# Performance work log

Measured on AMD Instinct MI355X. Metric: run time of the kernel, lower is better.

Reference implementation:

```python
import jax, jax.numpy as jnp
import numpy as np


def setup_inputs() -> dict:
    key = jax.random.key(0)
    k1, k2 = jax.random.split(key)
    B, C, H, W, K = 4, 3, 720, 1280, 5
    data = jax.random.normal(k1, (B, C, H, W), dtype=jnp.float32)
    kernels = jax.random.normal(k2, (B, K * K, H, W), dtype=jnp.float32)
    return {"data": data, "kernels": kernels}


def reference(data, kernels):
    # data: [B, C, H, W]; kernels: [B, K*K, H, W]
    bs, k2, h, w = kernels.shape
    k = int(np.sqrt(k2))
    r = k // 2
    # softmax-normalize the K*K weights per pixel (dim=1 in the torch module)
    kern = jax.nn.softmax(kernels, axis=1).reshape(bs, k, k, h, w)
    # zero-pad data so out-of-bound neighbors contribute 0 (matches skipped
    # out-of-range taps in the CUDA kernel_weighting op)
    pad = jnp.pad(data, ((0, 0), (0, 0), (r, r), (r, r)))
    out = jnp.zeros_like(data)
    # fixed small K*K loop (25 taps); each tap is a shifted slice * per-pixel weight
    for i in range(k):
        for j in range(k):
            out = out + pad[:, :, i:i + h, j:j + w] * kern[:, i, j][:, None, :, :]
    return out
```

## Files before the change

kernel.cpp:

```cpp
#include <hip/hip_runtime.h>
#include <math.h>

#define BB 4
#define CC 3
#define HH 720
#define WW 1280
#define KS 5
#define KK 25
#define RR 2

__global__ __launch_bounds__(256) void kpn_weighting_kernel(
    const float* __restrict__ data,
    const float* __restrict__ kern,
    float* __restrict__ out)
{
    const int HW = HH * WW;
    int idx = blockIdx.x * blockDim.x + threadIdx.x;
    const int total = BB * HW;
    if (idx >= total) return;

    int b  = idx / HW;
    int hw = idx - b * HW;
    int h  = hw / WW;
    int w  = hw - h * WW;

    const float* kp = kern + (size_t)b * KK * HW + hw;
    float wt[KK];
    float m = -1e30f;
    #pragma unroll
    for (int t = 0; t < KK; ++t) {
        wt[t] = kp[(size_t)t * HW];
        m = fmaxf(m, wt[t]);
    }
    float s = 0.f;
    #pragma unroll
    for (int t = 0; t < KK; ++t) {
        wt[t] = __expf(wt[t] - m);
        s += wt[t];
    }
    float inv = 1.0f / s;
    #pragma unroll
    for (int t = 0; t < KK; ++t) wt[t] *= inv;

    #pragma unroll
    for (int c = 0; c < CC; ++c) {
        const float* dp = data + ((size_t)b * CC + c) * HW;
        float acc = 0.f;
        #pragma unroll
        for (int i = 0; i < KS; ++i) {
            int hh = h + i - RR;
            if (hh < 0 || hh >= HH) continue;
            const float* rowp = dp + (size_t)hh * WW;
            #pragma unroll
            for (int j = 0; j < KS; ++j) {
                int ww = w + j - RR;
                if (ww < 0 || ww >= WW) continue;
                acc = fmaf(rowp[ww], wt[i * KS + j], acc);
            }
        }
        out[((size_t)b * CC + c) * HW + hw] = acc;
    }
}

extern "C" void kernel_launch(void* const* d_in, const int* in_sizes, int n_in,
                              void* d_out, int out_size, void* d_ws, size_t ws_size,
                              hipStream_t stream) {
    const float* data = (const float*)d_in[0];
    const float* kern = (const float*)d_in[1];
    float* out = (float*)d_out;

    const int total = BB * HH * WW;
    const int block = 256;
    const int grid = (total + block - 1) / block;
    kpn_weighting_kernel<<<grid, block, 0, stream>>>(data, kern, out);
}
```

Before: 626.4 us.

## Process four pixels per thread with float4 loads and nontemporal kernel streaming

Each thread now handles four adjacent output pixels. It loads the 25 softmax logits as float4 nontemporal loads and reads each data row as three float4 vectors covering a 12-wide window, with zero fill at the image edges. Outputs go out as nontemporal float4 stores. The aim is fewer, wider memory transactions on a bandwidth-bound stencil, and less cache pollution from the single-use kernel tensor, at the cost of higher register pressure (100 weight registers per thread) and a quarter as many threads.

```diff
diff --git a/kernel.cpp b/kernel.cpp
--- a/kernel.cpp
+++ b/kernel.cpp
@@ -8,57 +8,89 @@
 #define KS 5
 #define KK 25
 #define RR 2
+#define W4 (WW / 4)
+#define HW (HH * WW)
 
-__global__ __launch_bounds__(256) void kpn_weighting_kernel(
+typedef float f4 __attribute__((ext_vector_type(4)));
+
+__global__ __launch_bounds__(256) void kpn_weighting_v4(
     const float* __restrict__ data,
     const float* __restrict__ kern,
     float* __restrict__ out)
 {
-    const int HW = HH * WW;
-    int idx = blockIdx.x * blockDim.x + threadIdx.x;
-    const int total = BB * HW;
+    const int idx = blockIdx.x * blockDim.x + threadIdx.x;
+    const int total = BB * HH * W4;
     if (idx >= total) return;
 
-    int b  = idx / HW;
-    int hw = idx - b * HW;
-    int h  = hw / WW;
-    int w  = hw - h * WW;
+    const int b   = idx / (HH * W4);
+    const int rem = idx - b * (HH * W4);
+    const int h   = rem / W4;
+    const int w0  = (rem - h * W4) * 4;
 
-    const float* kp = kern + (size_t)b * KK * HW + hw;
-    float wt[KK];
-    float m = -1e30f;
+    const float* kp = kern + (size_t)b * KK * HW + (size_t)h * WW + w0;
+    f4 kw[KK];
     #pragma unroll
     for (int t = 0; t < KK; ++t) {
-        wt[t] = kp[(size_t)t * HW];
-        m = fmaxf(m, wt[t]);
+        kw[t] = __builtin_nontemporal_load((const f4*)(kp + (size_t)t * HW));
     }
-    float s = 0.f;
+
+    f4 m = kw[0];
+    #pragma unroll
+    for (int t = 1; t < KK; ++t) {
+        m.x = fmaxf(m.x, kw[t].x); m.y = fmaxf(m.y, kw[t].y);
+        m.z = fmaxf(m.z, kw[t].z); m.w = fmaxf(m.w, kw[t].w);
+    }
+    f4 s = {0.f, 0.f, 0.f, 0.f};
     #pragma unroll
     for (int t = 0; t < KK; ++t) {
-        wt[t] = __expf(wt[t] - m);
-        s += wt[t];
+        kw[t].x = __expf(kw[t].x - m.x); s.x += kw[t].x;
+        kw[t].y = __expf(kw[t].y - m.y); s.y += kw[t].y;
+        kw[t].z = __expf(kw[t].z - m.z); s.z += kw[t].z;
+        kw[t].w = __expf(kw[t].w - m.w); s.w += kw[t].w;
     }
-    float inv = 1.0f / s;
+    const f4 inv = {1.f / s.x, 1.f / s.y, 1.f / s.z, 1.f / s.w};
     #pragma unroll
-    for (int t = 0; t < KK; ++t) wt[t] *= inv;
+    for (int t = 0; t < KK; ++t) kw[t] *= inv;
 
     #pragma unroll
     for (int c = 0; c < CC; ++c) {
         const float* dp = data + ((size_t)b * CC + c) * HW;
-        float acc = 0.f;
+        f4 acc = {0.f, 0.f, 0.f, 0.f};
         #pragma unroll
         for (int i = 0; i < KS; ++i) {
-            int hh = h + i - RR;
+            const int hh = h + i - RR;
             if (hh < 0 || hh >= HH) continue;
-            const float* rowp = dp + (size_t)hh * WW;
+            const float* rp = dp + (size_t)hh * WW + w0;
+
+            float rb[12];
+            if (w0 >= 4) {
+                const f4 v = *(const f4*)(rp - 4);
+                rb[0] = v.x; rb[1] = v.y; rb[2] = v.z; rb[3] = v.w;
+            } else {
+                rb[0] = rb[1] = rb[2] = rb[3] = 0.f;
+            }
+            {
+                const f4 v = *(const f4*)rp;
+                rb[4] = v.x; rb[5] = v.y; rb[6] = v.z; rb[7] = v.w;
+            }
+            if (w0 + 7 < WW) {
+                const f4 v = *(const f4*)(rp + 4);
+                rb[8] = v.x; rb[9] = v.y; rb[10] = v.z; rb[11] = v.w;
+            } else {
+                rb[8] = rb[9] = rb[10] = rb[11] = 0.f;
+            }
+
             #pragma unroll
             for (int j = 0; j < KS; ++j) {
-                int ww = w + j - RR;
-                if (ww < 0 || ww >= WW) continue;
-                acc = fmaf(rowp[ww], wt[i * KS + j], acc);
+                const f4 wt = kw[i * KS + j];
+                acc.x = fmaf(rb[2 + j], wt.x, acc.x);
+                acc.y = fmaf(rb[3 + j], wt.y, acc.y);
+                acc.z = fmaf(rb[4 + j], wt.z, acc.z);
+                acc.w = fmaf(rb[5 + j], wt.w, acc.w);
             }
         }
-        out[((size_t)b * CC + c) * HW + hw] = acc;
+        __builtin_nontemporal_store(acc,
+            (f4*)(out + ((size_t)b * CC + c) * HW + (size_t)h * WW + w0));
     }
 }
 
@@ -69,8 +101,8 @@
     const float* kern = (const float*)d_in[1];
     float* out = (float*)d_out;
 
-    const int total = BB * HH * WW;
+    const int total = BB * HH * W4;
     const int block = 256;
     const int grid = (total + block - 1) / block;
-    kpn_weighting_kernel<<<grid, block, 0, stream>>>(data, kern, out);
+    kpn_weighting_v4<<<grid, block, 0, stream>>>(data, kern, out);
 }
```

Result: faster. 515.2 us (-17.7%).
